# Optimization experiments

Hardware: AMD Instinct MI355X
Metric: run time of the kernel (lower is better)

## Reference

```python
import jax, jax.numpy as jnp
import numpy as np

TEMPERATURE = 0.7
TOP_P = 0.9
TOP_K = 50
B, V = 128, 128000


def setup_inputs() -> dict:
    key = jax.random.key(0)
    k1, k2, k3 = jax.random.split(key, 3)
    logits = jax.random.normal(k1, (B, V), dtype=jnp.float32) * 3.0
    input_ids = jax.random.randint(k2, (B, 64), 0, V, dtype=jnp.int64)
    u = jax.random.uniform(k3, (B,), dtype=jnp.float32)
    return {"logits": logits, "input_ids": input_ids, "u": u}


def _warp_logits(logits):
    # TemperatureLogitsWarper
    x = logits / TEMPERATURE
    # TopPLogitsWarper (HF semantics): ascending sort, cumulative softmax,
    # remove tokens whose cumulative prob <= 1 - top_p; keep >= 1 token.
    order = jnp.argsort(x, axis=-1)                       # ascending
    sorted_x = jnp.take_along_axis(x, order, axis=-1)
    cum = jnp.cumsum(jax.nn.softmax(sorted_x, axis=-1), axis=-1)
    remove_sorted = cum <= (1.0 - TOP_P)
    remove_sorted = remove_sorted.at[..., -1:].set(False)  # min_tokens_to_keep=1
    inv = jnp.argsort(order, axis=-1)                     # inverse permutation
    remove = jnp.take_along_axis(remove_sorted, inv, axis=-1)
    x = jnp.where(remove, -jnp.inf, x)
    # TopKLogitsWarper: keep top_k, mask everything strictly below the k-th value
    kth = jax.lax.top_k(x, TOP_K)[0][..., -1:]
    x = jnp.where(x < kth, -jnp.inf, x)
    return x


def reference(logits, input_ids, u):
    # input_ids is unused in the warp path (repetition_penalty == 1.0)
    x = _warp_logits(logits)
    probs = jax.nn.softmax(x, axis=-1)                    # [B, V]
    # torch.multinomial(probs, 1) via inverse-CDF with uniform u
    cdf = jnp.cumsum(probs, axis=-1)
    token = jnp.argmax(cdf >= u[:, None], axis=-1)        # [B]
    return token
```

## Files before the change

### kernel.cpp

```cpp
#include <hip/hip_runtime.h>
#include <cmath>


constexpr int   NSEGA  = 64;
constexpr int   NSPLIT = 32;
constexpr int   BLK    = 256;
constexpr int   NBINS  = 1024;
constexpr int   BPL    = NBINS / 64;
constexpr int   TOPK   = 50;
constexpr float TEMP   = 0.7f;
constexpr float SPANC  = 5.0f;
constexpr int   CAPSEG = 128;
constexpr int   NCAND  = NSPLIT * CAPSEG;
constexpr int   BLK_F  = 256;
constexpr int   CAPC   = 128;
constexpr float LOG2E_OVER_T = (float)(1.4426950408889634 / 0.7);

__global__ __launch_bounds__(BLK)
void max_kernel(const float* __restrict__ logits, float* __restrict__ segmax,
                int V, int seglen)
{
  const int seg  = blockIdx.x;
  const int row  = blockIdx.y;
  const int tid  = threadIdx.x, lane = tid & 63, wave = tid >> 6;
  const int start = seg * seglen;
  const int len  = (V - start < seglen) ? (V - start) : seglen;

  __shared__ float red[BLK / 64];

  if (len <= 0) { if (tid == 0) segmax[row * NSEGA + seg] = -INFINITY; return; }

  const float* __restrict__ base = logits + (size_t)row * V + start;
  const bool vec4 = ((len & 3) == 0) && ((((size_t)base) & 15) == 0);
  const int len4 = vec4 ? (len >> 2) : 0;
  const float4* b4 = reinterpret_cast<const float4*>(base);

  float m = -INFINITY;
  {
    int i = tid;
    for (; i + BLK < len4; i += 2 * BLK) {
      float4 a = b4[i];
      float4 b = b4[i + BLK];
      m = fmaxf(m, fmaxf(fmaxf(a.x, a.y), fmaxf(a.z, a.w)));
      m = fmaxf(m, fmaxf(fmaxf(b.x, b.y), fmaxf(b.z, b.w)));
    }
    for (; i < len4; i += BLK) {
      float4 a = b4[i];
      m = fmaxf(m, fmaxf(fmaxf(a.x, a.y), fmaxf(a.z, a.w)));
    }
  }
  for (int i = (len4 << 2) + tid; i < len; i += BLK) m = fmaxf(m, base[i]);
  #pragma unroll
  for (int off = 32; off >= 1; off >>= 1) m = fmaxf(m, __shfl_xor(m, off, 64));
  if (lane == 0) red[wave] = m;
  __syncthreads();
  if (tid == 0) {
    float v = red[0];
    for (int w = 1; w < BLK / 64; ++w) v = fmaxf(v, red[w]);
    segmax[row * NSEGA + seg] = v;
  }
}

__global__ __launch_bounds__(BLK)
void zcol_kernel(const float* __restrict__ logits, const float* __restrict__ segmax,
                 float* __restrict__ segz,
                 float* __restrict__ cand_v, int* __restrict__ cand_i,
                 unsigned int* __restrict__ cnt16,
                 int V, int seglen)
{
  const int seg  = blockIdx.x;
  const int row  = blockIdx.y;
  const int tid  = threadIdx.x, lane = tid & 63, wave = tid >> 6;
  const int start = seg * seglen;
  const int len  = (V - start < seglen) ? (V - start) : seglen;

  __shared__ float red[BLK / 64];
  __shared__ unsigned int s_nf;
  __shared__ float bl_v[CAPSEG];
  __shared__ int   bl_i[CAPSEG];

  if (len <= 0) {
    if (tid == 0) { segz[row * NSPLIT + seg] = 0.f;
                    cnt16[row * NSPLIT + seg] = 0u; }
    return;
  }

  float sm = segmax[row * NSEGA + lane];
  #pragma unroll
  for (int off = 32; off >= 1; off >>= 1) sm = fmaxf(sm, __shfl_xor(sm, off, 64));
  const float M  = sm;
  const float lo = M - SPANC;

  if (tid == 0) s_nf = 0u;
  __syncthreads();

  const float* __restrict__ base = logits + (size_t)row * V + start;
  const bool vec4 = ((len & 3) == 0) && ((((size_t)base) & 15) == 0);
  const int len4 = vec4 ? (len >> 2) : 0;
  const float4* b4 = reinterpret_cast<const float4*>(base);

  float zs = 0.f;
  {
    int i = tid;
    for (; i + BLK < len4; i += 2 * BLK) {
      float4 a = b4[i];
      float4 b = b4[i + BLK];
      #pragma unroll
      for (int c = 0; c < 4; ++c) {
        float l = (c == 0) ? a.x : (c == 1) ? a.y : (c == 2) ? a.z : a.w;
        zs += exp2f((l - M) * LOG2E_OVER_T);
        if (l > lo) {
          unsigned int p = atomicAdd(&s_nf, 1u);
          if (p < CAPSEG) { bl_v[p] = l; bl_i[p] = start + (i << 2) + c; }
        }
      }
      #pragma unroll
      for (int c = 0; c < 4; ++c) {
        float l = (c == 0) ? b.x : (c == 1) ? b.y : (c == 2) ? b.z : b.w;
        zs += exp2f((l - M) * LOG2E_OVER_T);
        if (l > lo) {
          unsigned int p = atomicAdd(&s_nf, 1u);
          if (p < CAPSEG) { bl_v[p] = l; bl_i[p] = start + ((i + BLK) << 2) + c; }
        }
      }
    }
    for (; i < len4; i += BLK) {
      float4 a = b4[i];
      #pragma unroll
      for (int c = 0; c < 4; ++c) {
        float l = (c == 0) ? a.x : (c == 1) ? a.y : (c == 2) ? a.z : a.w;
        zs += exp2f((l - M) * LOG2E_OVER_T);
        if (l > lo) {
          unsigned int p = atomicAdd(&s_nf, 1u);
          if (p < CAPSEG) { bl_v[p] = l; bl_i[p] = start + (i << 2) + c; }
        }
      }
    }
  }
  for (int i = (len4 << 2) + tid; i < len; i += BLK) {
    float l = base[i];
    zs += exp2f((l - M) * LOG2E_OVER_T);
    if (l > lo) {
      unsigned int p = atomicAdd(&s_nf, 1u);
      if (p < CAPSEG) { bl_v[p] = l; bl_i[p] = start + i; }
    }
  }
  #pragma unroll
  for (int off = 32; off >= 1; off >>= 1) zs += __shfl_xor(zs, off, 64);
  if (lane == 0) red[wave] = zs;
  __syncthreads();

  if (tid == 0) {
    float v = red[0];
    for (int w = 1; w < BLK / 64; ++w) v += red[w];
    segz[row * NSPLIT + seg] = v;
  }
  unsigned int nf = s_nf; if (nf > CAPSEG) nf = CAPSEG;
  float* cvout = cand_v + ((size_t)row * NSPLIT + seg) * CAPSEG;
  int*   ciout = cand_i + ((size_t)row * NSPLIT + seg) * CAPSEG;
  for (unsigned int i = tid; i < nf; i += BLK) { cvout[i] = bl_v[i]; ciout[i] = bl_i[i]; }
  if (tid == 0) cnt16[row * NSPLIT + seg] = nf;
}

__global__ __launch_bounds__(BLK_F)
void finish_kernel(const float* __restrict__ segmax, const float* __restrict__ segz,
                   const float* __restrict__ cand_v, const int* __restrict__ cand_i,
                   const unsigned int* __restrict__ cnt16,
                   const float* __restrict__ uvec, int* __restrict__ out)
{
  const int row  = blockIdx.x;
  const int tid  = threadIdx.x;
  const int lane = tid & 63;

  __shared__ unsigned int hist[NBINS];
  __shared__ unsigned int chunk[64];
  __shared__ unsigned int cnt_s[NSPLIT];
  __shared__ float s_M, s_Z;
  __shared__ int   s_bstar;
  __shared__ unsigned int s_nc;
  __shared__ float fv[CAPC];
  __shared__ int   fi[CAPC];
  __shared__ float ov_[CAPC];
  __shared__ int   oi_[CAPC];
  __shared__ float eo[64];
  __shared__ float o2e[64];
  __shared__ int   o2i[64];
  __shared__ int   s_nk;

  if (tid < NSPLIT) cnt_s[tid] = cnt16[row * NSPLIT + tid];
  if (tid < 64) {
    float sm = segmax[row * NSEGA + lane];
    #pragma unroll
    for (int off = 32; off >= 1; off >>= 1) sm = fmaxf(sm, __shfl_xor(sm, off, 64));
    float zt = (lane < NSPLIT) ? segz[row * NSPLIT + lane] : 0.f;
    #pragma unroll
    for (int off = 32; off >= 1; off >>= 1) zt += __shfl_xor(zt, off, 64);
    if (lane == 0) { s_M = sm; s_Z = zt; s_nc = 0u; }
  }
  for (int i = tid; i < NBINS; i += BLK_F) hist[i] = 0u;
  __syncthreads();

  const float M  = s_M;
  const float lo = M - SPANC;
  const float binscale = (float)NBINS / SPANC;
  const float* cvrow = cand_v + (size_t)row * NCAND;
  const int*   cirow = cand_i + (size_t)row * NCAND;

  for (int i = tid; i < NCAND; i += BLK_F) {
    int sg = i >> 7;
    int ix = i & (CAPSEG - 1);
    if ((unsigned)ix < cnt_s[sg]) {
      float v = cvrow[i];
      int b = (int)((v - lo) * binscale);
      b = (b < 0) ? 0 : ((b > NBINS - 1) ? (NBINS - 1) : b);
      atomicAdd(&hist[b], 1u);
    }
  }
  __syncthreads();

  if (tid < 64) {
    unsigned int csum = 0;
    const int cb = tid * BPL;
    #pragma unroll
    for (int j = 0; j < BPL; ++j) csum += hist[cb + j];
    chunk[tid] = csum;
  }
  __syncthreads();
  if (tid < 64) {
    unsigned int csum = chunk[tid];
    unsigned int suf = 0;
    for (int l2 = 0; l2 < 64; ++l2) {
      unsigned int c2 = chunk[l2];
      suf += (l2 >= tid) ? c2 : 0u;
    }
    unsigned long long bal = __ballot(suf >= (unsigned)TOPK);
    if (bal == 0ull) {
      if (tid == 0) s_bstar = 0;
    } else {
      int L = 63 - __builtin_clzll(bal);
      if (tid == L) {
        unsigned int running = suf - csum;
        const int cb = tid * BPL;
        unsigned int h[BPL];
        #pragma unroll
        for (int j = 0; j < BPL; ++j) h[j] = hist[cb + j];
        int bsel = cb;
        #pragma unroll
        for (int j = BPL - 1; j >= 0; --j) {
          running += h[j];
          if (running >= (unsigned)TOPK) { bsel = cb + j; break; }
        }
        s_bstar = bsel;
      }
    }
  }
  __syncthreads();

  const int bstar = s_bstar;
  for (int i = tid; i < NCAND; i += BLK_F) {
    int sg = i >> 7;
    int ix = i & (CAPSEG - 1);
    if ((unsigned)ix < cnt_s[sg]) {
      float v = cvrow[i];
      int b = (int)((v - lo) * binscale);
      b = (b < 0) ? 0 : ((b > NBINS - 1) ? (NBINS - 1) : b);
      if (b >= bstar) {
        unsigned int p = atomicAdd(&s_nc, 1u);
        if (p < CAPC) { fv[p] = v; fi[p] = cirow[i]; }
      }
    }
  }
  __syncthreads();

  const int ns = ((int)s_nc < CAPC) ? (int)s_nc : CAPC;
  if (tid < 64) {
    float c0v = (lane < ns)      ? fv[lane]      : 0.f;
    int   c0i = (lane < ns)      ? fi[lane]      : 0;
    float c1v = (lane + 64 < ns) ? fv[lane + 64] : 0.f;
    int   c1i = (lane + 64 < ns) ? fi[lane + 64] : 0;
    int r0 = 0, r1 = 0;
    for (int j = 0; j < ns; ++j) {
      float vj = fv[j]; int ij = fi[j];
      if (vj > c0v || (vj == c0v && ij < c0i)) ++r0;
      if (vj > c1v || (vj == c1v && ij < c1i)) ++r1;
    }
    if (lane < ns)      { ov_[r0] = c0v; oi_[r0] = c0i; }
    if (lane + 64 < ns) { ov_[r1] = c1v; oi_[r1] = c1i; }
  }
  __syncthreads();

  const float Mx = M / TEMP;
  if (tid < 64 && lane < ns && lane < TOPK) {
    float x = ov_[lane] / TEMP;
    eo[lane] = expf(x - Mx);
  }
  __syncthreads();

  if (tid == 0) {
    const float thresh = 0.9f * s_Z;
    const int nkmax = (ns < TOPK) ? ns : TOPK;
    float cum = 0.f; int nk = 0;
    for (int k = 0; k < TOPK; ++k) {
      float ek = eo[k];
      bool take = (k < nkmax) && (cum < thresh);
      if (take) { cum += ek; nk++; }
    }
    s_nk = nk;
  }
  __syncthreads();

  const int nk = s_nk;
  if (tid < 64 && lane < nk) {
    int myi = oi_[lane];
    int rank = 0;
    for (int j = 0; j < nk; ++j) rank += (oi_[j] < myi) ? 1 : 0;
    o2e[rank] = eo[lane]; o2i[rank] = myi;
  }
  __syncthreads();

  if (tid == 0) {
    float S = 0.f;
    for (int j = 0; j < nk; ++j) S += o2e[j];
    const float uu = uvec[row];
    float c = 0.f; int token = 0; int found = 0;
    for (int j = 0; j < nk; ++j) {
      float q = o2e[j] / S;
      c += q;
      if (!found && c >= uu) { token = o2i[j]; found = 1; }
    }
    out[row] = token;
  }
}

extern "C" void kernel_launch(void* const* d_in, const int* in_sizes, int n_in,
                              void* d_out, int out_size, void* d_ws, size_t ws_size,
                              hipStream_t stream) {
  const float* logits = (const float*)d_in[0];
  const float* u = (const float*)d_in[2];
  int* out = (int*)d_out;
  const int B = in_sizes[2];
  const int V = in_sizes[0] / B;
  int seglenA = (V + NSEGA - 1) / NSEGA;  seglenA = (seglenA + 3) & ~3;
  int seglenB = (V + NSPLIT - 1) / NSPLIT; seglenB = (seglenB + 3) & ~3;

  char* ws = (char*)d_ws;
  float* segmax = (float*)ws;
  float* segz   = segmax + (size_t)B * NSEGA;
  unsigned int* cnt16 = (unsigned int*)(segz + (size_t)B * NSPLIT);
  float* cand_v = (float*)(cnt16 + (size_t)B * NSPLIT);
  int*   cand_i = (int*)(cand_v + (size_t)B * NCAND);

  max_kernel<<<dim3(NSEGA, B), dim3(BLK), 0, stream>>>(logits, segmax, V, seglenA);
  zcol_kernel<<<dim3(NSPLIT, B), dim3(BLK), 0, stream>>>(
      logits, segmax, segz, cand_v, cand_i, cnt16, V, seglenB);
  finish_kernel<<<dim3(B), dim3(BLK_F), 0, stream>>>(
      segmax, segz, cand_v, cand_i, cnt16, u, out);
}
```

Baseline: 55.78 us.

## Fuse max pass into single online-softmax candidate collection kernel

Replaces the separate max kernel and the normalizer/candidate kernel with one pass that tracks a running per-segment max per tile, rescaling the partial sum as in online softmax. Candidates are collected against the running local max rather than the global max, so segment capacity is raised from 128 to 512. The finish kernel combines per-segment maxima and rescales the partial sums. This halves reads of the logits and drops a launch, in exchange for two block barriers per tile, more candidate traffic, and possible early overcollection that could overflow capacity.

```diff
diff --git a/kernel.cpp b/kernel.cpp
--- a/kernel.cpp
+++ b/kernel.cpp
@@ -2,22 +2,26 @@
 #include <cmath>
 
 
-constexpr int   NSEGA  = 64;
 constexpr int   NSPLIT = 32;
 constexpr int   BLK    = 256;
+constexpr int   TILE4  = BLK * 4;
 constexpr int   NBINS  = 1024;
 constexpr int   BPL    = NBINS / 64;
 constexpr int   TOPK   = 50;
 constexpr float TEMP   = 0.7f;
+constexpr float SPANS  = 5.0f;
 constexpr float SPANC  = 5.0f;
-constexpr int   CAPSEG = 128;
+constexpr int   CAPSEG = 512;
 constexpr int   NCAND  = NSPLIT * CAPSEG;
 constexpr int   BLK_F  = 256;
 constexpr int   CAPC   = 128;
 constexpr float LOG2E_OVER_T = (float)(1.4426950408889634 / 0.7);
 
 __global__ __launch_bounds__(BLK)
-void max_kernel(const float* __restrict__ logits, float* __restrict__ segmax,
+void zmc_kernel(const float* __restrict__ logits,
+                float* __restrict__ segmax, float* __restrict__ segz,
+                float* __restrict__ cand_v, int* __restrict__ cand_i,
+                unsigned int* __restrict__ cnt16,
                 int V, int seglen)
 {
   const int seg  = blockIdx.x;
@@ -27,133 +31,107 @@
   const int len  = (V - start < seglen) ? (V - start) : seglen;
 
   __shared__ float red[BLK / 64];
-
-  if (len <= 0) { if (tid == 0) segmax[row * NSEGA + seg] = -INFINITY; return; }
-
-  const float* __restrict__ base = logits + (size_t)row * V + start;
-  const bool vec4 = ((len & 3) == 0) && ((((size_t)base) & 15) == 0);
-  const int len4 = vec4 ? (len >> 2) : 0;
-  const float4* b4 = reinterpret_cast<const float4*>(base);
-
-  float m = -INFINITY;
-  {
-    int i = tid;
-    for (; i + BLK < len4; i += 2 * BLK) {
-      float4 a = b4[i];
-      float4 b = b4[i + BLK];
-      m = fmaxf(m, fmaxf(fmaxf(a.x, a.y), fmaxf(a.z, a.w)));
-      m = fmaxf(m, fmaxf(fmaxf(b.x, b.y), fmaxf(b.z, b.w)));
-    }
-    for (; i < len4; i += BLK) {
-      float4 a = b4[i];
-      m = fmaxf(m, fmaxf(fmaxf(a.x, a.y), fmaxf(a.z, a.w)));
-    }
-  }
-  for (int i = (len4 << 2) + tid; i < len; i += BLK) m = fmaxf(m, base[i]);
-  #pragma unroll
-  for (int off = 32; off >= 1; off >>= 1) m = fmaxf(m, __shfl_xor(m, off, 64));
-  if (lane == 0) red[wave] = m;
-  __syncthreads();
-  if (tid == 0) {
-    float v = red[0];
-    for (int w = 1; w < BLK / 64; ++w) v = fmaxf(v, red[w]);
-    segmax[row * NSEGA + seg] = v;
-  }
-}
-
-__global__ __launch_bounds__(BLK)
-void zcol_kernel(const float* __restrict__ logits, const float* __restrict__ segmax,
-                 float* __restrict__ segz,
-                 float* __restrict__ cand_v, int* __restrict__ cand_i,
-                 unsigned int* __restrict__ cnt16,
-                 int V, int seglen)
-{
-  const int seg  = blockIdx.x;
-  const int row  = blockIdx.y;
-  const int tid  = threadIdx.x, lane = tid & 63, wave = tid >> 6;
-  const int start = seg * seglen;
-  const int len  = (V - start < seglen) ? (V - start) : seglen;
-
-  __shared__ float red[BLK / 64];
+  __shared__ float s_bm;
   __shared__ unsigned int s_nf;
   __shared__ float bl_v[CAPSEG];
   __shared__ int   bl_i[CAPSEG];
 
   if (len <= 0) {
-    if (tid == 0) { segz[row * NSPLIT + seg] = 0.f;
-                    cnt16[row * NSPLIT + seg] = 0u; }
+    if (tid == 0) { segmax[row * NSPLIT + seg] = -INFINITY;
+                    segz  [row * NSPLIT + seg] = 0.f;
+                    cnt16 [row * NSPLIT + seg] = 0u; }
     return;
   }
-
-  float sm = segmax[row * NSEGA + lane];
-  #pragma unroll
-  for (int off = 32; off >= 1; off >>= 1) sm = fmaxf(sm, __shfl_xor(sm, off, 64));
-  const float M  = sm;
-  const float lo = M - SPANC;
-
   if (tid == 0) s_nf = 0u;
   __syncthreads();
 
   const float* __restrict__ base = logits + (size_t)row * V + start;
-  const bool vec4 = ((len & 3) == 0) && ((((size_t)base) & 15) == 0);
-  const int len4 = vec4 ? (len >> 2) : 0;
+  const int len4 = len >> 2;
+  const int tail = len & 3;
   const float4* b4 = reinterpret_cast<const float4*>(base);
 
+  float mb = -INFINITY;
   float zs = 0.f;
-  {
-    int i = tid;
-    for (; i + BLK < len4; i += 2 * BLK) {
-      float4 a = b4[i];
-      float4 b = b4[i + BLK];
+  const int ntiles = (len4 + TILE4 - 1) / TILE4;
+
+  for (int t = 0; t < ntiles; ++t) {
+    const int tb = t * TILE4;
+    float4 r[4];
+    #pragma unroll
+    for (int u = 0; u < 4; ++u) {
+      int i4 = tb + u * BLK + tid;
+      r[u] = (i4 < len4) ? b4[i4]
+                         : make_float4(-INFINITY, -INFINITY, -INFINITY, -INFINITY);
+    }
+    float tm = -INFINITY;
+    #pragma unroll
+    for (int u = 0; u < 4; ++u)
+      tm = fmaxf(tm, fmaxf(fmaxf(r[u].x, r[u].y), fmaxf(r[u].z, r[u].w)));
+    #pragma unroll
+    for (int off = 32; off >= 1; off >>= 1) tm = fmaxf(tm, __shfl_xor(tm, off, 64));
+    if (lane == 0) red[wave] = tm;
+    __syncthreads();
+    if (tid == 0) {
+      float v = red[0];
+      for (int w = 1; w < BLK / 64; ++w) v = fmaxf(v, red[w]);
+      s_bm = v;
+    }
+    __syncthreads();
+    const float mnew = fmaxf(mb, s_bm);
+    if (mnew > mb) zs *= exp2f((mb - mnew) * LOG2E_OVER_T);
+    mb = mnew;
+    const float lo = mb - SPANS;
+
+    #pragma unroll
+    for (int u = 0; u < 4; ++u) {
+      const int i4 = tb + u * BLK + tid;
       #pragma unroll
       for (int c = 0; c < 4; ++c) {
-        float l = (c == 0) ? a.x : (c == 1) ? a.y : (c == 2) ? a.z : a.w;
-        zs += exp2f((l - M) * LOG2E_OVER_T);
+        float l = (c == 0) ? r[u].x : (c == 1) ? r[u].y : (c == 2) ? r[u].z : r[u].w;
+        zs += exp2f((l - mb) * LOG2E_OVER_T);
         if (l > lo) {
           unsigned int p = atomicAdd(&s_nf, 1u);
-          if (p < CAPSEG) { bl_v[p] = l; bl_i[p] = start + (i << 2) + c; }
+          if (p < CAPSEG) { bl_v[p] = l; bl_i[p] = start + (i4 << 2) + c; }
         }
       }
-      #pragma unroll
-      for (int c = 0; c < 4; ++c) {
-        float l = (c == 0) ? b.x : (c == 1) ? b.y : (c == 2) ? b.z : b.w;
-        zs += exp2f((l - M) * LOG2E_OVER_T);
-        if (l > lo) {
-          unsigned int p = atomicAdd(&s_nf, 1u);
-          if (p < CAPSEG) { bl_v[p] = l; bl_i[p] = start + ((i + BLK) << 2) + c; }
-        }
-      }
-    }
-    for (; i < len4; i += BLK) {
-      float4 a = b4[i];
-      #pragma unroll
-      for (int c = 0; c < 4; ++c) {
-        float l = (c == 0) ? a.x : (c == 1) ? a.y : (c == 2) ? a.z : a.w;
-        zs += exp2f((l - M) * LOG2E_OVER_T);
-        if (l > lo) {
-          unsigned int p = atomicAdd(&s_nf, 1u);
-          if (p < CAPSEG) { bl_v[p] = l; bl_i[p] = start + (i << 2) + c; }
-        }
-      }
-    }
-  }
-  for (int i = (len4 << 2) + tid; i < len; i += BLK) {
-    float l = base[i];
-    zs += exp2f((l - M) * LOG2E_OVER_T);
-    if (l > lo) {
+    }
+    __syncthreads();
+  }
+
+  if (tail) {
+    const int idx = (len4 << 2) + tid;
+    float l = (idx < len) ? base[idx] : -INFINITY;
+    float tm = l;
+    #pragma unroll
+    for (int off = 32; off >= 1; off >>= 1) tm = fmaxf(tm, __shfl_xor(tm, off, 64));
+    if (lane == 0) red[wave] = tm;
+    __syncthreads();
+    if (tid == 0) {
+      float v = red[0];
+      for (int w = 1; w < BLK / 64; ++w) v = fmaxf(v, red[w]);
+      s_bm = v;
+    }
+    __syncthreads();
+    const float mnew = fmaxf(mb, s_bm);
+    if (mnew > mb) zs *= exp2f((mb - mnew) * LOG2E_OVER_T);
+    mb = mnew;
+    zs += exp2f((l - mb) * LOG2E_OVER_T);
+    if (l > mb - SPANS) {
       unsigned int p = atomicAdd(&s_nf, 1u);
-      if (p < CAPSEG) { bl_v[p] = l; bl_i[p] = start + i; }
-    }
-  }
+      if (p < CAPSEG) { bl_v[p] = l; bl_i[p] = start + idx; }
+    }
+    __syncthreads();
+  }
+
   #pragma unroll
   for (int off = 32; off >= 1; off >>= 1) zs += __shfl_xor(zs, off, 64);
   if (lane == 0) red[wave] = zs;
   __syncthreads();
-
   if (tid == 0) {
     float v = red[0];
     for (int w = 1; w < BLK / 64; ++w) v += red[w];
-    segz[row * NSPLIT + seg] = v;
+    segz  [row * NSPLIT + seg] = v;
+    segmax[row * NSPLIT + seg] = mb;
   }
   unsigned int nf = s_nf; if (nf > CAPSEG) nf = CAPSEG;
   float* cvout = cand_v + ((size_t)row * NSPLIT + seg) * CAPSEG;
@@ -171,6 +149,7 @@
   const int row  = blockIdx.x;
   const int tid  = threadIdx.x;
   const int lane = tid & 63;
+  const float invT = 1.0f / TEMP;
 
   __shared__ unsigned int hist[NBINS];
   __shared__ unsigned int chunk[64];
@@ -189,13 +168,14 @@
 
   if (tid < NSPLIT) cnt_s[tid] = cnt16[row * NSPLIT + tid];
   if (tid < 64) {
-    float sm = segmax[row * NSEGA + lane];
-    #pragma unroll
-    for (int off = 32; off >= 1; off >>= 1) sm = fmaxf(sm, __shfl_xor(sm, off, 64));
-    float zt = (lane < NSPLIT) ? segz[row * NSPLIT + lane] : 0.f;
+    float sm = (lane < NSPLIT) ? segmax[row * NSPLIT + lane] : -INFINITY;
+    float m = sm;
+    #pragma unroll
+    for (int off = 32; off >= 1; off >>= 1) m = fmaxf(m, __shfl_xor(m, off, 64));
+    float zt = (lane < NSPLIT) ? segz[row * NSPLIT + lane] * expf((sm - m) * invT) : 0.f;
     #pragma unroll
     for (int off = 32; off >= 1; off >>= 1) zt += __shfl_xor(zt, off, 64);
-    if (lane == 0) { s_M = sm; s_Z = zt; s_nc = 0u; }
+    if (lane == 0) { s_M = m; s_Z = zt; s_nc = 0u; }
   }
   for (int i = tid; i < NBINS; i += BLK_F) hist[i] = 0u;
   __syncthreads();
@@ -207,7 +187,7 @@
   const int*   cirow = cand_i + (size_t)row * NCAND;
 
   for (int i = tid; i < NCAND; i += BLK_F) {
-    int sg = i >> 7;
+    int sg = i >> 9;
     int ix = i & (CAPSEG - 1);
     if ((unsigned)ix < cnt_s[sg]) {
       float v = cvrow[i];
@@ -258,7 +238,7 @@
 
   const int bstar = s_bstar;
   for (int i = tid; i < NCAND; i += BLK_F) {
-    int sg = i >> 7;
+    int sg = i >> 9;
     int ix = i & (CAPSEG - 1);
     if ((unsigned)ix < cnt_s[sg]) {
       float v = cvrow[i];
@@ -340,19 +320,18 @@
   int* out = (int*)d_out;
   const int B = in_sizes[2];
   const int V = in_sizes[0] / B;
-  int seglenA = (V + NSEGA - 1) / NSEGA;  seglenA = (seglenA + 3) & ~3;
-  int seglenB = (V + NSPLIT - 1) / NSPLIT; seglenB = (seglenB + 3) & ~3;
+  int seglen = (V + NSPLIT - 1) / NSPLIT;
+  seglen = (seglen + 3) & ~3;
 
   char* ws = (char*)d_ws;
   float* segmax = (float*)ws;
-  float* segz   = segmax + (size_t)B * NSEGA;
+  float* segz   = segmax + (size_t)B * NSPLIT;
   unsigned int* cnt16 = (unsigned int*)(segz + (size_t)B * NSPLIT);
   float* cand_v = (float*)(cnt16 + (size_t)B * NSPLIT);
   int*   cand_i = (int*)(cand_v + (size_t)B * NCAND);
 
-  max_kernel<<<dim3(NSEGA, B), dim3(BLK), 0, stream>>>(logits, segmax, V, seglenA);
-  zcol_kernel<<<dim3(NSPLIT, B), dim3(BLK), 0, stream>>>(
-      logits, segmax, segz, cand_v, cand_i, cnt16, V, seglenB);
+  zmc_kernel<<<dim3(NSPLIT, B), dim3(BLK), 0, stream>>>(
+      logits, segmax, segz, cand_v, cand_i, cnt16, V, seglen);
   finish_kernel<<<dim3(B), dim3(BLK_F), 0, stream>>>(
       segmax, segz, cand_v, cand_i, cnt16, u, out);
 }
```

Measured after the change: 62.25 us. 11.6% more time.
